# Kernel tuning notes

Measured on AMD Instinct MI355X. Metric: run time of the kernel, lower is better.

The kernel has to match this reference:

```python
import jax, jax.numpy as jnp
import numpy as np

B, S, C = 16, 2048, 512
E = S            # embed_dim == seq_len (RMSNorm applied on transposed seq axis)
H = 4 * E        # FFN hidden
LAMBDA_INIT = float(0.8 - 0.6 * np.exp(-0.3 * 1.0))  # layer_index = 1
SCALE = E ** (-0.25)
K = 5            # decomposition moving-average kernel


def rmsnorm(x, w, eps=1e-8):
    return x * jax.lax.rsqrt(jnp.mean(x * x, axis=-1, keepdims=True) + eps) * w


def decompose(a):
    # DLinear-style series decomposition: replicate-padded moving average along seq
    pad = (K - 1) // 2
    ap = jnp.concatenate([jnp.repeat(a[:, :1], pad, axis=1), a, jnp.repeat(a[:, -1:], pad, axis=1)], axis=1)
    n = a.shape[1]
    trend = sum(ap[:, i:i + n] for i in range(K)) / K
    return trend, a - trend


def setup_inputs() -> dict:
    key = jax.random.key(0)
    ks = jax.random.split(key, 12)
    p = lambda i, shape, s=0.02: jax.random.normal(ks[i], shape, jnp.float32) * s
    return {
        "x": jax.random.normal(ks[0], (B, S, C), jnp.float32),
        "ln_attn_w": jnp.ones((E,), jnp.float32),
        "q12_w": p(1, (E, 2 * E)), "q12_b": jnp.zeros((2 * E,), jnp.float32),
        "k12_w": p(2, (E, 2 * E)), "k12_b": jnp.zeros((2 * E,), jnp.float32),
        "v_w": p(3, (E, E)), "v_b": jnp.zeros((E,), jnp.float32),
        "lambda_q1": p(4, (E,), 0.1), "lambda_k1": p(5, (E,), 0.1),
        "lambda_q2": p(6, (E,), 0.1), "lambda_k2": p(7, (E,), 0.1),
        "norm_w": jnp.ones((E,), jnp.float32),
        "ln_ff_w": jnp.ones((E,), jnp.float32),
        "ff_w1": p(8, (E, H)), "ff_b1": jnp.zeros((H,), jnp.float32),
        "ff_w2": p(9, (H, E)), "ff_b2": jnp.zeros((E,), jnp.float32),
    }


def reference(x, ln_attn_w, q12_w, q12_b, k12_w, k12_b, v_w, v_b,
              lambda_q1, lambda_k1, lambda_q2, lambda_k2,
              norm_w, ln_ff_w, ff_w1, ff_b1, ff_w2, ff_b2):
    # pre-attention RMSNorm over the seq axis (via transpose)
    a = jnp.swapaxes(rmsnorm(jnp.swapaxes(x, -1, -2), ln_attn_w), -1, -2)  # [B,S,C]
    trend, seasonal = decompose(a)
    # project seq dim of trend/seasonal (iTransformer style: channels are tokens)
    q = jnp.swapaxes(trend, -1, -2) @ q12_w + q12_b      # [B,C,2S]
    q1, q2 = jnp.split(q, 2, axis=-1)                    # [B,C,S] each
    k = jnp.swapaxes(seasonal, -1, -2) @ k12_w + k12_b   # [B,C,2S]
    k1, k2 = jnp.split(k, 2, axis=-1)                    # [B,C,S]
    v = jnp.swapaxes(a, -1, -2) @ v_w + v_b              # [B,C,S]
    a1 = jnp.einsum('bis,bjs->bij', q1, k1) * SCALE      # [B,C,C]
    a2 = jnp.einsum('bis,bjs->bij', q2, k2) * SCALE      # [B,C,C]
    lam = jnp.exp(jnp.sum(lambda_q1 * lambda_k1)) - jnp.exp(jnp.sum(lambda_q2 * lambda_k2)) + LAMBDA_INIT
    d = jax.nn.softmax(a1, axis=-1) - lam * jax.nn.softmax(a2, axis=-1)
    attn = rmsnorm(d @ v, norm_w) * (1.0 - LAMBDA_INIT)  # [B,C,S]
    x = x + jnp.swapaxes(attn, -1, -2)
    # FFN over the seq axis
    h = rmsnorm(jnp.swapaxes(x, -1, -2), ln_ff_w)        # [B,C,S]
    ff = jax.nn.gelu(h @ ff_w1 + ff_b1, approximate=False) @ ff_w2 + ff_b2
    return x + jnp.swapaxes(ff, -1, -2)
```

## Files before the change

### kernel.cpp

```cpp
#include <hip/hip_runtime.h>
#include <hip/hip_bf16.h>

#define B_ 16
#define S_ 2048
#define C_ 512
#define H_ 8192

#define LAMBDA_INIT_F 0.3555090675909693f
#define ONE_M_LI_F    0.6444909324090307f
#define SCALE_F       0.14865088937534013f

using bf16x8 = __attribute__((ext_vector_type(8))) short;
using f32x4  = __attribute__((ext_vector_type(4))) float;

__device__ __forceinline__ float b2f(ushort u) {
  union { unsigned u; float f; } x; x.u = ((unsigned)u) << 16; return x.f;
}
__device__ __forceinline__ ushort f2b(float f) {
  union { float f; unsigned u; } x; x.f = f;
  unsigned r = x.u + 0x7fffu + ((x.u >> 16) & 1u);
  return (ushort)(r >> 16);
}

__device__ __forceinline__ void load_lds16(const void* g, void* s) {
  __builtin_amdgcn_global_load_lds((const __attribute__((address_space(1))) void*)g,
                                   (__attribute__((address_space(3))) void*)s,
                                   16, 0, 0);
}

#define WAITV8() asm volatile("s_waitcnt vmcnt(8)" ::: "memory")
#define WAITV4() asm volatile("s_waitcnt vmcnt(4)" ::: "memory")
#define WAITV0() asm volatile("s_waitcnt vmcnt(0)" ::: "memory")
#define WAITL0() do { asm volatile("s_waitcnt lgkmcnt(0)" ::: "memory"); __builtin_amdgcn_sched_barrier(0); } while (0)
#define BAR()    __builtin_amdgcn_s_barrier()

template <int EPI>
__global__ __launch_bounds__(512, 1) void gemm256(
    const ushort* __restrict__ A, const ushort* __restrict__ Bt,
    ushort* __restrict__ C, const float* __restrict__ bias,
    const ushort* __restrict__ addm,
    int K, int lda, int ldb, int ldc)
{
  __shared__ ushort lds[65536];
  const int t = threadIdx.x, w = t >> 6, lane = t & 63;
  const int fr = lane & 15, khl = lane >> 4;
  const int wr = w >> 2, wc = w & 3;

  const int gx = gridDim.x;
  const int id = blockIdx.y * gx + blockIdx.x;
  const int nwg = gx * gridDim.y;
  const int swz = (id & 7) * (nwg >> 3) + (id >> 3);
  const int m0 = (swz % gx) * 256, n0 = (swz / gx) * 256;

  const int sl    = (t & 7) ^ ((t >> 3) & 7);
  const int rbase = ((t >> 3) << 1) + (sl >> 2);
  const int khs   = sl & 3;
  const size_t aoff = (size_t)(m0 + rbase) * lda + khs * 8;
  const size_t boff = (size_t)(n0 + rbase) * ldb + khs * 8;
  const size_t jstA = (size_t)128 * lda, jstB = (size_t)128 * ldb;

  int ao[8], bo[4];
#pragma unroll
  for (int m = 0; m < 8; ++m) {
    const int row = wr * 128 + m * 16 + fr, dr = row >> 1;
    const int so = (((row & 1) << 2) + khl) ^ (dr & 7);
    ao[m] = dr * 64 + so * 8;
  }
#pragma unroll
  for (int n = 0; n < 4; ++n) {
    const int row = wc * 64 + n * 16 + fr, dr = row >> 1;
    const int so = (((row & 1) << 2) + khl) ^ (dr & 7);
    bo[n] = 8192 + dr * 64 + so * 8;
  }

  f32x4 acc[8][4] = {};
  const int U = K >> 5;

#define STAGE_U(u) do { \
    const ushort* sa_ = A  + aoff + (size_t)(u) * 32; \
    const ushort* sb_ = Bt + boff + (size_t)(u) * 32; \
    ushort* da_ = &lds[((u) & 3) * 16384 + w * 512]; \
    load_lds16(sa_, da_); load_lds16(sa_ + jstA, da_ + 4096); \
    load_lds16(sb_, da_ + 8192); load_lds16(sb_ + jstB, da_ + 12288); } while (0)
#define LDFRAG(u) do { const int sb_ = ((u) & 3) * 16384; \
    _Pragma("unroll") for (int m_ = 0; m_ < 8; ++m_) af[m_] = *(const bf16x8*)&lds[sb_ + ao[m_]]; \
    _Pragma("unroll") for (int n_ = 0; n_ < 4; ++n_) bg[n_] = *(const bf16x8*)&lds[sb_ + bo[n_]]; } while (0)
#define MFMA32() do { __builtin_amdgcn_s_setprio(1); \
    _Pragma("unroll") for (int m_ = 0; m_ < 8; ++m_) \
    _Pragma("unroll") for (int n_ = 0; n_ < 4; ++n_) \
      acc[m_][n_] = __builtin_amdgcn_mfma_f32_16x16x32_bf16(af[m_], bg[n_], acc[m_][n_], 0, 0, 0); \
    __builtin_amdgcn_s_setprio(0); } while (0)

  STAGE_U(0); STAGE_U(1); STAGE_U(2);
  WAITV8(); BAR();

  bf16x8 af[8], bg[4];
#pragma unroll 4
  for (int u = 0; u <= U - 4; ++u) {
    LDFRAG(u);
    STAGE_U(u + 3);
    WAITL0();
    MFMA32();
    WAITV8();
    BAR();
  }
  {
    LDFRAG(U - 3);
    WAITL0();
    MFMA32();
    WAITV4();
    BAR();
  }
  {
    LDFRAG(U - 2);
    WAITL0();
    MFMA32();
    WAITV0();
    BAR();
  }
  {
    LDFRAG(U - 1);
    WAITL0();
    MFMA32();
  }
#undef STAGE_U
#undef LDFRAG
#undef MFMA32

  const int r0 = khl * 4;
#pragma unroll
  for (int m = 0; m < 8; ++m)
#pragma unroll
    for (int nf = 0; nf < 4; ++nf) {
      const int gr = m0 + wr * 128 + m * 16 + r0;
      const int gc = n0 + wc * 64 + nf * 16 + fr;
      const float bb = (EPI == 3) ? 0.f : bias[gc];
#pragma unroll
      for (int r = 0; r < 4; ++r) {
        const size_t idx = (size_t)(gr + r) * ldc + gc;
        float v = acc[m][nf][r];
        if constexpr (EPI == 1) v += bb;
        if constexpr (EPI == 2) { v += bb; v = 0.5f * v * (1.f + erff(v * 0.7071067811865475f)); }
        if constexpr (EPI == 4) v += bb + b2f(addm[idx]) + b2f(C[idx]);
        C[idx] = f2b(v);
      }
    }
}

template <int EPI>
__global__ __launch_bounds__(256, 2) void gemm_nt(
    const ushort* __restrict__ Aall, const ushort* __restrict__ Ball,
    void* __restrict__ Call, int K, int lda, int ldb, int ldc,
    long sA, long sB, long sC, long sA2, long sB2, float alpha)
{
  __shared__ ushort lA[4096];
  __shared__ ushort lB[4096];
  const int t = threadIdx.x;
  const int m0 = blockIdx.x * 128, n0 = blockIdx.y * 128;
  const int zb = blockIdx.z & 15, zh = blockIdx.z >> 4;
  const ushort* A  = Aall + (size_t)zb * sA + (size_t)zh * sA2;
  const ushort* Bt = Ball + (size_t)zb * sB + (size_t)zh * sB2;
  const int lane = t & 63;
  const int wave = t >> 6;
  const int wm = (wave >> 1) * 64, wn = (wave & 1) * 64;
  const int fr = lane & 15, kh = lane >> 4;
  f32x4 acc[4][4] = {};
  const int srow = t >> 2;
  const int scol = (t & 3) * 8;
  const size_t ar0 = (size_t)(m0 + srow) * lda + scol;
  const size_t ar1 = (size_t)(m0 + 64 + srow) * lda + scol;
  const size_t br0 = (size_t)(n0 + srow) * ldb + scol;
  const size_t br1 = (size_t)(n0 + 64 + srow) * ldb + scol;
  const int wbase = wave * 512;

  for (int k0 = 0; k0 < K; k0 += 32) {
    __syncthreads();
    load_lds16(A + ar0 + k0,  &lA[wbase]);
    load_lds16(A + ar1 + k0,  &lA[2048 + wbase]);
    load_lds16(Bt + br0 + k0, &lB[wbase]);
    load_lds16(Bt + br1 + k0, &lB[2048 + wbase]);
    __syncthreads();
    bf16x8 af[4], bg[4];
#pragma unroll
    for (int i = 0; i < 4; ++i)
      af[i] = *(const bf16x8*)&lA[(wm + i * 16 + fr) * 32 + kh * 8];
#pragma unroll
    for (int j = 0; j < 4; ++j)
      bg[j] = *(const bf16x8*)&lB[(wn + j * 16 + fr) * 32 + kh * 8];
#pragma unroll
    for (int i = 0; i < 4; ++i)
#pragma unroll
      for (int j = 0; j < 4; ++j)
        acc[i][j] = __builtin_amdgcn_mfma_f32_16x16x32_bf16(af[i], bg[j], acc[i][j], 0, 0, 0);
  }

  const int r0 = kh * 4;
  if constexpr (EPI == 0) {
    float* C = (float*)Call + (size_t)blockIdx.z * sC;
#pragma unroll
    for (int i = 0; i < 4; ++i)
#pragma unroll
      for (int j = 0; j < 4; ++j) {
        const int gr = m0 + wm + i * 16 + r0;
        const int gc = n0 + wn + j * 16 + fr;
#pragma unroll
        for (int r = 0; r < 4; ++r)
          C[(size_t)(gr + r) * ldc + gc] = acc[i][j][r] * alpha;
      }
  } else {
    ushort* C = (ushort*)Call + (size_t)blockIdx.z * sC;
#pragma unroll
    for (int i = 0; i < 4; ++i)
#pragma unroll
      for (int j = 0; j < 4; ++j) {
        const int gr = m0 + wm + i * 16 + r0;
        const int gc = n0 + wn + j * 16 + fr;
#pragma unroll
        for (int r = 0; r < 4; ++r)
          C[(size_t)(gr + r) * ldc + gc] = f2b(acc[i][j][r] * alpha);
      }
  }
}

__device__ __forceinline__ float block_sum(float v, float* red) {
#pragma unroll
  for (int o = 32; o > 0; o >>= 1) v += __shfl_down(v, o, 64);
  __syncthreads();
  if ((threadIdx.x & 63) == 0) red[threadIdx.x >> 6] = v;
  __syncthreads();
  return red[0] + red[1] + red[2] + red[3];
}
__device__ __forceinline__ float block_max(float v, float* red) {
#pragma unroll
  for (int o = 32; o > 0; o >>= 1) v = fmaxf(v, __shfl_down(v, o, 64));
  __syncthreads();
  if ((threadIdx.x & 63) == 0) red[threadIdx.x >> 6] = v;
  __syncthreads();
  return fmaxf(fmaxf(red[0], red[1]), fmaxf(red[2], red[3]));
}

__global__ __launch_bounds__(256) void k_rms_part(const float* __restrict__ x, float* __restrict__ part) {
  const int c = blockIdx.x * 256 + threadIdx.x;
  const int sl = blockIdx.y;
  const int b = blockIdx.z;
  const float* p = x + (size_t)b * S_ * C_ + c;
  const int s0 = sl * 256;
  float s = 0.f;
  for (int i = 0; i < 256; ++i) { float v = p[(size_t)(s0 + i) * C_]; s += v * v; }
  part[((size_t)b * C_ + c) * 8 + sl] = s;
}
__global__ __launch_bounds__(256) void k_rms_fin(const float* __restrict__ part, float* __restrict__ rms1) {
  const int i = blockIdx.x * 256 + threadIdx.x;
  const float* p = part + (size_t)i * 8;
  float s = 0.f;
#pragma unroll
  for (int j = 0; j < 8; ++j) s += p[j];
  rms1[i] = rsqrtf(s * (1.f / S_) + 1e-8f);
}

__global__ __launch_bounds__(256) void k_trans_norm(const float* __restrict__ x, const float* __restrict__ rms1,
                                                    const float* __restrict__ w,
                                                    ushort* __restrict__ aT, ushort* __restrict__ xT) {
  __shared__ float tile[32][33];
  const int s0 = blockIdx.x * 32, c0 = blockIdx.y * 32, b = blockIdx.z;
  const int tx = threadIdx.x, ty = threadIdx.y;
  const float* xb = x + (size_t)b * S_ * C_;
#pragma unroll
  for (int r = 0; r < 4; ++r) {
    const int s = ty + 8 * r;
    tile[s][tx] = xb[(size_t)(s0 + s) * C_ + c0 + tx];
  }
  __syncthreads();
#pragma unroll
  for (int r = 0; r < 4; ++r) {
    const int c = ty + 8 * r;
    const float v = tile[tx][c];
    const float rm = rms1[b * C_ + c0 + c];
    const size_t o = ((size_t)b * C_ + c0 + c) * S_ + s0 + tx;
    xT[o] = f2b(v);
    aT[o] = f2b(v * rm * w[s0 + tx]);
  }
}

__global__ __launch_bounds__(256) void k_wtrans(const float* __restrict__ W, ushort* __restrict__ WT,
                                                int Kd, int Ndstride, int n_base) {
  __shared__ float tile[32][33];
  const int k0 = blockIdx.x * 32, n0 = blockIdx.y * 32;
  const int tx = threadIdx.x, ty = threadIdx.y;
#pragma unroll
  for (int r = 0; r < 4; ++r) {
    const int k = ty + 8 * r;
    tile[k][tx] = W[(size_t)(k0 + k) * Ndstride + n_base + n0 + tx];
  }
  __syncthreads();
#pragma unroll
  for (int r = 0; r < 4; ++r) {
    const int n = ty + 8 * r;
    WT[(size_t)(n0 + n) * Kd + k0 + tx] = f2b(tile[tx][n]);
  }
}

__global__ __launch_bounds__(256) void k_bt(const ushort* __restrict__ in, ushort* __restrict__ out, int R, int CL) {
  __shared__ ushort tile[32][33];
  const int r0 = blockIdx.x * 32, c0 = blockIdx.y * 32;
  const size_t zb = (size_t)blockIdx.z * R * CL;
  const int tx = threadIdx.x, ty = threadIdx.y;
#pragma unroll
  for (int r = 0; r < 4; ++r) {
    const int rr = ty + 8 * r;
    tile[rr][tx] = in[zb + (size_t)(r0 + rr) * CL + c0 + tx];
  }
  __syncthreads();
#pragma unroll
  for (int r = 0; r < 4; ++r) {
    const int cc = ty + 8 * r;
    out[zb + (size_t)(c0 + cc) * R + r0 + tx] = tile[tx][cc];
  }
}

__device__ __forceinline__ float trend5(const ushort* p, int s) {
  float sum = 0.f;
#pragma unroll
  for (int d = -2; d <= 2; ++d) {
    int ss = s + d; ss = ss < 0 ? 0 : (ss > S_ - 1 ? S_ - 1 : ss);
    sum += b2f(p[ss]);
  }
  return sum * 0.2f;
}
__global__ __launch_bounds__(256) void k_dtrend(const ushort* __restrict__ aT, ushort* __restrict__ trT) {
  const size_t i = (size_t)blockIdx.x * 256 + threadIdx.x;
  const int s = (int)(i & (S_ - 1));
  trT[i] = f2b(trend5(aT + (i - s), s));
}
__global__ __launch_bounds__(256) void k_dseason(const ushort* __restrict__ aT, ushort* __restrict__ seT) {
  const size_t i = (size_t)blockIdx.x * 256 + threadIdx.x;
  const int s = (int)(i & (S_ - 1));
  const ushort* p = aT + (i - s);
  seT[i] = f2b(b2f(p[s]) - trend5(p, s));
}

__global__ __launch_bounds__(256) void k_lambda(const float* __restrict__ lq1, const float* __restrict__ lk1,
                                                const float* __restrict__ lq2, const float* __restrict__ lk2,
                                                float* __restrict__ lam) {
  __shared__ float r1[4], r2[4];
  const int t = threadIdx.x;
  float s1 = 0.f, s2 = 0.f;
  for (int i = t; i < S_; i += 256) { s1 += lq1[i] * lk1[i]; s2 += lq2[i] * lk2[i]; }
#pragma unroll
  for (int o = 32; o > 0; o >>= 1) { s1 += __shfl_down(s1, o, 64); s2 += __shfl_down(s2, o, 64); }
  if ((t & 63) == 0) { r1[t >> 6] = s1; r2[t >> 6] = s2; }
  __syncthreads();
  if (t == 0) {
    const float a = r1[0] + r1[1] + r1[2] + r1[3];
    const float b = r2[0] + r2[1] + r2[2] + r2[3];
    *lam = expf(a) - expf(b) + LAMBDA_INIT_F;
  }
}

__global__ __launch_bounds__(256) void k_softmax(const float* __restrict__ a1, const float* __restrict__ a2,
                                                 const float* __restrict__ lamp, ushort* __restrict__ dm) {
  __shared__ float red[4];
  const size_t row = blockIdx.x;
  const float* p1 = a1 + row * 512;
  const float* p2 = a2 + row * 512;
  const int t = threadIdx.x;
  const float v1a = p1[t], v1b = p1[t + 256];
  const float v2a = p2[t], v2b = p2[t + 256];
  const float m1 = block_max(fmaxf(v1a, v1b), red);
  const float m2 = block_max(fmaxf(v2a, v2b), red);
  const float e1a = expf(v1a - m1), e1b = expf(v1b - m1);
  const float e2a = expf(v2a - m2), e2b = expf(v2b - m2);
  const float s1 = block_sum(e1a + e1b, red);
  const float s2 = block_sum(e2a + e2b, red);
  const float i1 = 1.f / s1, i2 = (*lamp) / s2;
  ushort* o = dm + row * 512;
  o[t]       = f2b(e1a * i1 - e2a * i2);
  o[t + 256] = f2b(e1b * i1 - e2b * i2);
}

__global__ __launch_bounds__(256) void k_postattn(const ushort* __restrict__ P, const ushort* __restrict__ xT,
                                                  const float* __restrict__ norm_w, const float* __restrict__ ln_ff_w,
                                                  ushort* __restrict__ attn, ushort* __restrict__ h) {
  __shared__ float red[4];
  const size_t row = blockIdx.x;
  const ushort* p = P + row * S_;
  const int t = threadIdx.x;
  float v[8]; float ss = 0.f;
#pragma unroll
  for (int i = 0; i < 8; ++i) { v[i] = b2f(p[t + 256 * i]); ss += v[i] * v[i]; }
  ss = block_sum(ss, red);
  const float inv = rsqrtf(ss * (1.f / S_) + 1e-8f);
  const ushort* xr = xT + row * S_;
  ushort* ar = attn + row * S_;
  float x2[8]; float ss2 = 0.f;
#pragma unroll
  for (int i = 0; i < 8; ++i) {
    const int s = t + 256 * i;
    const float at = v[i] * inv * norm_w[s] * ONE_M_LI_F;
    ar[s] = f2b(at);
    const float xx = b2f(xr[s]) + at;
    x2[i] = xx; ss2 += xx * xx;
  }
  ss2 = block_sum(ss2, red);
  const float inv2 = rsqrtf(ss2 * (1.f / S_) + 1e-8f);
  ushort* hr = h + row * S_;
#pragma unroll
  for (int i = 0; i < 8; ++i) { const int s = t + 256 * i; hr[s] = f2b(x2[i] * inv2 * ln_ff_w[s]); }
}

__global__ __launch_bounds__(256) void k_final2(const float* __restrict__ x, const ushort* __restrict__ sumT,
                                                float* __restrict__ out) {
  __shared__ float tile[32][33];
  const int s0 = blockIdx.x * 32, c0 = blockIdx.y * 32, b = blockIdx.z;
  const int tx = threadIdx.x, ty = threadIdx.y;
#pragma unroll
  for (int r = 0; r < 4; ++r) {
    const int c = ty + 8 * r;
    tile[c][tx] = b2f(sumT[((size_t)b * C_ + c0 + c) * S_ + s0 + tx]);
  }
  __syncthreads();
#pragma unroll
  for (int r = 0; r < 4; ++r) {
    const int s = ty + 8 * r;
    const size_t o = ((size_t)b * S_ + s0 + s) * C_ + c0 + tx;
    out[o] = x[o] + tile[tx][s];
  }
}

__global__ void k_probe(float* out, float v) { out[0] = v; }

extern "C" void kernel_launch(void* const* d_in, const int* in_sizes, int n_in,
                              void* d_out, int out_size, void* d_ws, size_t ws_size,
                              hipStream_t stream) {
  const float* x       = (const float*)d_in[0];
  const float* ln_attn = (const float*)d_in[1];
  const float* q12_w   = (const float*)d_in[2];
  const float* q12_b   = (const float*)d_in[3];
  const float* k12_w   = (const float*)d_in[4];
  const float* k12_b   = (const float*)d_in[5];
  const float* v_w     = (const float*)d_in[6];
  const float* v_b     = (const float*)d_in[7];
  const float* lq1     = (const float*)d_in[8];
  const float* lk1     = (const float*)d_in[9];
  const float* lq2     = (const float*)d_in[10];
  const float* lk2     = (const float*)d_in[11];
  const float* norm_w  = (const float*)d_in[12];
  const float* ln_ff   = (const float*)d_in[13];
  const float* ff_w1   = (const float*)d_in[14];
  const float* ff_b1   = (const float*)d_in[15];
  const float* ff_w2   = (const float*)d_in[16];
  const float* ff_b2   = (const float*)d_in[17];
  float* out = (float*)d_out;

  if (ws_size < 184844544ull) {
    k_probe<<<1, 1, 0, stream>>>(out, (float)(ws_size >> 20));
    return;
  }

  char* ws = (char*)d_ws;
  ushort* slotA = (ushort*)(ws + 0);
  ushort* slotB = (ushort*)(ws + 33554432);
  ushort* slotC = (ushort*)(ws + 67108864);
  ushort* slotD = (ushort*)(ws + 100663296);
  ushort* slotE = (ushort*)(ws + 134217728);
  ushort* slotF = (ushort*)(ws + 167772160);
  float*  part  = (float*) (ws + 184549376);
  float*  rms1  = (float*) (ws + 184811520);
  float*  lamp  = (float*) (ws + 184844288);

  ushort* aT   = slotA;
  ushort* xT   = slotE;
  ushort* Vm   = slotB;
  ushort* VT   = slotD;
  ushort* trT  = slotB;
  ushort* seT  = slotC;
  ushort* K12  = slotA;
  float*  scr  = (float*)slotC;
  ushort* Pm   = slotB;
  ushort* attn = slotC;
  ushort* hbuf = slotA;
  ushort* ff1T = slotB;
  ushort* ff2T = slotD;
  ushort* ffo  = slotE;
  ushort* wsl  = slotF;
  ushort* dmat = slotF;
  ushort* Qm   = (ushort*)d_out;
  ushort* H1   = (ushort*)d_out;

  const dim3 blk256(256), blk512(512), blkT(32, 8);

  k_rms_part<<<dim3(2, 8, B_), blk256, 0, stream>>>(x, part);
  k_rms_fin<<<dim3(32), blk256, 0, stream>>>(part, rms1);
  k_trans_norm<<<dim3(64, 16, B_), blkT, 0, stream>>>(x, rms1, ln_attn, aT, xT);

  k_wtrans<<<dim3(64, 64), blkT, 0, stream>>>(v_w, wsl, 2048, 2048, 0);
  gemm256<1><<<dim3(32, 8), blk512, 0, stream>>>(aT, wsl, Vm, v_b, nullptr, 2048, 2048, 2048, 2048);
  k_bt<<<dim3(16, 64, B_), blkT, 0, stream>>>(Vm, VT, 512, 2048);

  k_dtrend<<<dim3(65536), blk256, 0, stream>>>(aT, trT);
  k_wtrans<<<dim3(64, 128), blkT, 0, stream>>>(q12_w, wsl, 2048, 4096, 0);
  gemm256<1><<<dim3(32, 16), blk512, 0, stream>>>(trT, wsl, Qm, q12_b, nullptr, 2048, 2048, 2048, 4096);

  k_dseason<<<dim3(65536), blk256, 0, stream>>>(aT, seT);
  k_lambda<<<dim3(1), blk256, 0, stream>>>(lq1, lk1, lq2, lk2, lamp);
  k_wtrans<<<dim3(64, 128), blkT, 0, stream>>>(k12_w, wsl, 2048, 4096, 0);
  gemm256<1><<<dim3(32, 16), blk512, 0, stream>>>(seT, wsl, K12, k12_b, nullptr, 2048, 2048, 2048, 4096);

  gemm_nt<0><<<dim3(4, 4, 32), blk256, 0, stream>>>(Qm, K12, scr, 2048, 4096, 4096, 512,
                                                    512L * 4096, 512L * 4096, 512L * 512,
                                                    2048L, 2048L, SCALE_F);

  k_softmax<<<dim3(8192), blk256, 0, stream>>>(scr, scr + 4194304, lamp, dmat);
  gemm_nt<3><<<dim3(4, 16, B_), blk256, 0, stream>>>(dmat, VT, Pm, 512, 512, 512, 2048,
                                                     512L * 512, 2048L * 512, 512L * 2048,
                                                     0, 0, 1.f);

  k_postattn<<<dim3(8192), blk256, 0, stream>>>(Pm, xT, norm_w, ln_ff, attn, hbuf);

  k_wtrans<<<dim3(64, 256), blkT, 0, stream>>>(ff_w1, ff1T, 2048, 8192, 0);
  k_wtrans<<<dim3(256, 64), blkT, 0, stream>>>(ff_w2, ff2T, 8192, 2048, 0);

  gemm256<2><<<dim3(32, 16), blk512, 0, stream>>>(hbuf, ff1T, H1, ff_b1, nullptr,
                                                  2048, 2048, 2048, 4096);
  gemm256<3><<<dim3(32, 8), blk512, 0, stream>>>(H1, ff2T, ffo, nullptr, nullptr,
                                                 4096, 4096, 8192, 2048);
  gemm256<2><<<dim3(32, 16), blk512, 0, stream>>>(hbuf, ff1T + (size_t)4096 * 2048, H1,
                                                  ff_b1 + 4096, nullptr, 2048, 2048, 2048, 4096);
  gemm256<4><<<dim3(32, 8), blk512, 0, stream>>>(H1, ff2T + 4096, ffo, ff_b2, attn,
                                                 4096, 4096, 8192, 2048);

  k_final2<<<dim3(64, 16, B_), blkT, 0, stream>>>(x, ffo, out);
}
```

Before: 1.297 ms.

## Double-buffer B fragments to prefetch next K-step LDS reads during MFMAs

Splits the LDS fragment loads into A and B parts and keeps two B-fragment register sets, so the B fragments for step u+1 are read while the MFMAs of step u run. The main loop is manually unrolled by two, with a wait on all but the last 4 LDS ops, and a tighter vmcnt(4) wait is used before each barrier. The aim is to hide LDS read latency behind matrix math. The cost is extra register pressure, and the loop assumes an even iteration structure and correct lgkmcnt accounting.

```diff
diff --git a/kernel.cpp b/kernel.cpp
--- a/kernel.cpp
+++ b/kernel.cpp
@@ -28,9 +28,9 @@
                                    16, 0, 0);
 }
 
-#define WAITV8() asm volatile("s_waitcnt vmcnt(8)" ::: "memory")
 #define WAITV4() asm volatile("s_waitcnt vmcnt(4)" ::: "memory")
 #define WAITV0() asm volatile("s_waitcnt vmcnt(0)" ::: "memory")
+#define WAITL4() do { asm volatile("s_waitcnt lgkmcnt(4)" ::: "memory"); __builtin_amdgcn_sched_barrier(0); } while (0)
 #define WAITL0() do { asm volatile("s_waitcnt lgkmcnt(0)" ::: "memory"); __builtin_amdgcn_sched_barrier(0); } while (0)
 #define BAR()    __builtin_amdgcn_s_barrier()
 
@@ -82,49 +82,65 @@
     ushort* da_ = &lds[((u) & 3) * 16384 + w * 512]; \
     load_lds16(sa_, da_); load_lds16(sa_ + jstA, da_ + 4096); \
     load_lds16(sb_, da_ + 8192); load_lds16(sb_ + jstB, da_ + 12288); } while (0)
-#define LDFRAG(u) do { const int sb_ = ((u) & 3) * 16384; \
-    _Pragma("unroll") for (int m_ = 0; m_ < 8; ++m_) af[m_] = *(const bf16x8*)&lds[sb_ + ao[m_]]; \
-    _Pragma("unroll") for (int n_ = 0; n_ < 4; ++n_) bg[n_] = *(const bf16x8*)&lds[sb_ + bo[n_]]; } while (0)
-#define MFMA32() do { __builtin_amdgcn_s_setprio(1); \
+#define LDA8(u) do { const int sb_ = ((u) & 3) * 16384; \
+    _Pragma("unroll") for (int m_ = 0; m_ < 8; ++m_) af[m_] = *(const bf16x8*)&lds[sb_ + ao[m_]]; } while (0)
+#define LDB4(u, dst) do { const int sb_ = ((u) & 3) * 16384; \
+    _Pragma("unroll") for (int n_ = 0; n_ < 4; ++n_) dst[n_] = *(const bf16x8*)&lds[sb_ + bo[n_]]; } while (0)
+#define MFMA32(bgv) do { __builtin_amdgcn_s_setprio(1); \
     _Pragma("unroll") for (int m_ = 0; m_ < 8; ++m_) \
     _Pragma("unroll") for (int n_ = 0; n_ < 4; ++n_) \
-      acc[m_][n_] = __builtin_amdgcn_mfma_f32_16x16x32_bf16(af[m_], bg[n_], acc[m_][n_], 0, 0, 0); \
+      acc[m_][n_] = __builtin_amdgcn_mfma_f32_16x16x32_bf16(af[m_], bgv[n_], acc[m_][n_], 0, 0, 0); \
     __builtin_amdgcn_s_setprio(0); } while (0)
 
+  bf16x8 af[8], bg0[4], bg1[4];
+
   STAGE_U(0); STAGE_U(1); STAGE_U(2);
-  WAITV8(); BAR();
-
-  bf16x8 af[8], bg[4];
-#pragma unroll 4
-  for (int u = 0; u <= U - 4; ++u) {
-    LDFRAG(u);
+  WAITV4(); BAR();
+  LDB4(0, bg0);
+
+  for (int u = 0; u <= U - 6; u += 2) {
+    LDA8(u);
     STAGE_U(u + 3);
+    LDB4(u + 1, bg1);
+    WAITL4();
+    MFMA32(bg0);
+    WAITV4(); BAR();
+    LDA8(u + 1);
+    STAGE_U(u + 4);
+    LDB4(u + 2, bg0);
+    WAITL4();
+    MFMA32(bg1);
+    WAITV4(); BAR();
+  }
+  {
+    LDA8(U - 4);
+    STAGE_U(U - 1);
+    LDB4(U - 3, bg1);
+    WAITL4();
+    MFMA32(bg0);
+    WAITV4(); BAR();
+  }
+  {
+    LDA8(U - 3);
+    LDB4(U - 2, bg0);
+    WAITL4();
+    MFMA32(bg1);
+    WAITV0(); BAR();
+  }
+  {
+    LDA8(U - 2);
+    LDB4(U - 1, bg1);
+    WAITL4();
+    MFMA32(bg0);
+  }
+  {
+    LDA8(U - 1);
     WAITL0();
-    MFMA32();
-    WAITV8();
-    BAR();
-  }
-  {
-    LDFRAG(U - 3);
-    WAITL0();
-    MFMA32();
-    WAITV4();
-    BAR();
-  }
-  {
-    LDFRAG(U - 2);
-    WAITL0();
-    MFMA32();
-    WAITV0();
-    BAR();
-  }
-  {
-    LDFRAG(U - 1);
-    WAITL0();
-    MFMA32();
+    MFMA32(bg1);
   }
 #undef STAGE_U
-#undef LDFRAG
+#undef LDA8
+#undef LDB4
 #undef MFMA32
 
   const int r0 = khl * 4;
```

Result: no change. 1.299 ms (+0.2%).

## Restructure GEMM main loop into 8-wave ping-pong with 64-wide K tiles

Applied to the files above, without the earlier changes.

Replaces the 4-stage, 32-wide-K pipeline in the 256x256 GEMM with a two-buffer scheme using 64-wide K slices. Each slice's compute is split into four quadrant MFMA groups, with global-to-LDS loads for the next tiles interleaved between quadrants and separated by barriers. The aim is finer-grained overlap of memory traffic and matrix math, plus fewer LDS fragment reloads via register reuse across quadrants. It adds many more barriers per iteration and requires K to be a multiple of 128.

```diff
diff --git a/kernel.cpp b/kernel.cpp
--- a/kernel.cpp
+++ b/kernel.cpp
@@ -28,7 +28,6 @@
                                    16, 0, 0);
 }
 
-#define WAITV8() asm volatile("s_waitcnt vmcnt(8)" ::: "memory")
 #define WAITV4() asm volatile("s_waitcnt vmcnt(4)" ::: "memory")
 #define WAITV0() asm volatile("s_waitcnt vmcnt(0)" ::: "memory")
 #define WAITL0() do { asm volatile("s_waitcnt lgkmcnt(0)" ::: "memory"); __builtin_amdgcn_sched_barrier(0); } while (0)
@@ -52,80 +51,93 @@
   const int swz = (id & 7) * (nwg >> 3) + (id >> 3);
   const int m0 = (swz % gx) * 256, n0 = (swz / gx) * 256;
 
-  const int sl    = (t & 7) ^ ((t >> 3) & 7);
-  const int rbase = ((t >> 3) << 1) + (sl >> 2);
-  const int khs   = sl & 3;
-  const size_t aoff = (size_t)(m0 + rbase) * lda + khs * 8;
-  const size_t boff = (size_t)(n0 + rbase) * ldb + khs * 8;
-  const size_t jstA = (size_t)128 * lda, jstB = (size_t)128 * ldb;
-
-  int ao[8], bo[4];
-#pragma unroll
-  for (int m = 0; m < 8; ++m) {
-    const int row = wr * 128 + m * 16 + fr, dr = row >> 1;
-    const int so = (((row & 1) << 2) + khl) ^ (dr & 7);
-    ao[m] = dr * 64 + so * 8;
-  }
-#pragma unroll
-  for (int n = 0; n < 4; ++n) {
-    const int row = wc * 64 + n * 16 + fr, dr = row >> 1;
-    const int so = (((row & 1) << 2) + khl) ^ (dr & 7);
-    bo[n] = 8192 + dr * 64 + so * 8;
-  }
+  const int cs0 = (khl ^ (fr & 7)) * 8;
+  const int cs1 = ((4 + khl) ^ (fr & 7)) * 8;
+  const int rowA = wr * 8192 + fr * 64;
+  const int rowB = 16384 + (wc >> 1) * 8192 + ((wc & 1) * 64 + fr) * 64;
+
+  const int srow = w * 8 + (lane >> 3);
+  const int scol = ((lane & 7) ^ ((lane >> 3) & 7)) * 8;
+  const int sR   = w * 512;
 
   f32x4 acc[8][4] = {};
-  const int U = K >> 5;
-
-#define STAGE_U(u) do { \
-    const ushort* sa_ = A  + aoff + (size_t)(u) * 32; \
-    const ushort* sb_ = Bt + boff + (size_t)(u) * 32; \
-    ushort* da_ = &lds[((u) & 3) * 16384 + w * 512]; \
-    load_lds16(sa_, da_); load_lds16(sa_ + jstA, da_ + 4096); \
-    load_lds16(sb_, da_ + 8192); load_lds16(sb_ + jstB, da_ + 12288); } while (0)
-#define LDFRAG(u) do { const int sb_ = ((u) & 3) * 16384; \
-    _Pragma("unroll") for (int m_ = 0; m_ < 8; ++m_) af[m_] = *(const bf16x8*)&lds[sb_ + ao[m_]]; \
-    _Pragma("unroll") for (int n_ = 0; n_ < 4; ++n_) bg[n_] = *(const bf16x8*)&lds[sb_ + bo[n_]]; } while (0)
-#define MFMA32() do { __builtin_amdgcn_s_setprio(1); \
-    _Pragma("unroll") for (int m_ = 0; m_ < 8; ++m_) \
-    _Pragma("unroll") for (int n_ = 0; n_ < 4; ++n_) \
-      acc[m_][n_] = __builtin_amdgcn_mfma_f32_16x16x32_bf16(af[m_], bg[n_], acc[m_][n_], 0, 0, 0); \
+  bf16x8 a[4][2], b[4][2];
+
+#define STG(P, grow, ld, kt, RG) do { \
+    const ushort* s0_ = (P) + (size_t)((grow) + srow) * (ld) + (kt) + scol; \
+    load_lds16(s0_, &lds[(RG) + sR]); \
+    load_lds16(s0_ + (size_t)64 * (ld), &lds[(RG) + 4096 + sR]); } while (0)
+#define LDA4(buf, mh) do { _Pragma("unroll") for (int m_ = 0; m_ < 4; ++m_) { \
+    a[m_][0] = *(const bf16x8*)&lds[(buf) + rowA + ((mh) * 4 + m_) * 1024 + cs0]; \
+    a[m_][1] = *(const bf16x8*)&lds[(buf) + rowA + ((mh) * 4 + m_) * 1024 + cs1]; } } while (0)
+#define LDB2(buf, nh) do { _Pragma("unroll") for (int n_ = 0; n_ < 2; ++n_) { \
+    b[(nh) * 2 + n_][0] = *(const bf16x8*)&lds[(buf) + rowB + ((nh) * 2 + n_) * 1024 + cs0]; \
+    b[(nh) * 2 + n_][1] = *(const bf16x8*)&lds[(buf) + rowB + ((nh) * 2 + n_) * 1024 + cs1]; } } while (0)
+#define Q16(mh, nh) do { __builtin_amdgcn_s_setprio(1); \
+    _Pragma("unroll") for (int ks_ = 0; ks_ < 2; ++ks_) \
+    _Pragma("unroll") for (int m_ = 0; m_ < 4; ++m_) \
+    _Pragma("unroll") for (int n_ = 0; n_ < 2; ++n_) \
+      acc[(mh) * 4 + m_][(nh) * 2 + n_] = __builtin_amdgcn_mfma_f32_16x16x32_bf16( \
+          a[m_][ks_], b[(nh) * 2 + n_][ks_], acc[(mh) * 4 + m_][(nh) * 2 + n_], 0, 0, 0); \
     __builtin_amdgcn_s_setprio(0); } while (0)
 
-  STAGE_U(0); STAGE_U(1); STAGE_U(2);
-  WAITV8(); BAR();
-
-  bf16x8 af[8], bg[4];
-#pragma unroll 4
-  for (int u = 0; u <= U - 4; ++u) {
-    LDFRAG(u);
-    STAGE_U(u + 3);
-    WAITL0();
-    MFMA32();
-    WAITV8();
-    BAR();
+  STG(Bt, n0,       ldb, 0,  16384);
+  STG(Bt, n0 + 128, ldb, 0,  24576);
+  STG(A,  m0,       lda, 0,  0);
+  STG(A,  m0 + 128, lda, 0,  8192);
+  STG(Bt, n0,       ldb, 64, 32768 + 16384);
+  STG(Bt, n0 + 128, ldb, 64, 32768 + 24576);
+  WAITV4(); BAR();
+
+  const int NI = K >> 7;
+  int kA = 0;
+#pragma unroll 1
+  for (int i = 0; i < NI - 1; ++i, kA += 128) {
+    LDA4(0, 0); LDB2(0, 0);
+    STG(A, m0, lda, kA + 64, 32768);
+    BAR(); WAITL0(); Q16(0, 0); BAR();
+    LDB2(0, 1);
+    STG(A, m0 + 128, lda, kA + 64, 32768 + 8192);
+    BAR(); WAITL0(); Q16(0, 1); BAR();
+    LDA4(0, 1);
+    STG(Bt, n0, ldb, kA + 128, 16384);
+    BAR(); WAITL0(); Q16(1, 1); BAR();
+    STG(Bt, n0 + 128, ldb, kA + 128, 24576);
+    BAR(); Q16(1, 0); WAITV4(); BAR();
+    LDA4(32768, 0); LDB2(32768, 0);
+    STG(A, m0, lda, kA + 128, 0);
+    BAR(); WAITL0(); Q16(0, 0); BAR();
+    LDB2(32768, 1);
+    STG(A, m0 + 128, lda, kA + 128, 8192);
+    BAR(); WAITL0(); Q16(0, 1); BAR();
+    LDA4(32768, 1);
+    STG(Bt, n0, ldb, kA + 192, 32768 + 16384);
+    BAR(); WAITL0(); Q16(1, 1); BAR();
+    STG(Bt, n0 + 128, ldb, kA + 192, 32768 + 24576);
+    BAR(); Q16(1, 0); WAITV4(); BAR();
   }
   {
-    LDFRAG(U - 3);
-    WAITL0();
-    MFMA32();
-    WAITV4();
-    BAR();
-  }
-  {
-    LDFRAG(U - 2);
-    WAITL0();
-    MFMA32();
-    WAITV0();
-    BAR();
-  }
-  {
-    LDFRAG(U - 1);
-    WAITL0();
-    MFMA32();
-  }
-#undef STAGE_U
-#undef LDFRAG
-#undef MFMA32
+    LDA4(0, 0); LDB2(0, 0);
+    STG(A, m0, lda, kA + 64, 32768);
+    BAR(); WAITL0(); Q16(0, 0); BAR();
+    LDB2(0, 1);
+    STG(A, m0 + 128, lda, kA + 64, 32768 + 8192);
+    BAR(); WAITL0(); Q16(0, 1); BAR();
+    LDA4(0, 1);
+    BAR(); WAITL0(); Q16(1, 1); BAR();
+    Q16(1, 0); WAITV0(); BAR();
+    LDA4(32768, 0); LDB2(32768, 0);
+    WAITL0(); Q16(0, 0);
+    LDB2(32768, 1);
+    WAITL0(); Q16(0, 1);
+    LDA4(32768, 1);
+    WAITL0(); Q16(1, 1);
+    Q16(1, 0);
+  }
+#undef STG
+#undef LDA4
+#undef LDB2
+#undef Q16
 
   const int r0 = khl * 4;
 #pragma unroll
```

Measured after the change: 1.401 ms. 1.08x slower.
